# Kernel optimization log

Hardware: AMD Instinct MI355X
Metric: run time of the kernel (lower is better)

## Reference

```python
import jax, jax.numpy as jnp
import numpy as np

B, T, C, H = 4, 2048, 1024, 16
D = C // H  # head_dim = 64


def setup_inputs() -> dict:
    key = jax.random.key(0)
    k1, k2, k3, k4 = jax.random.split(key, 4)
    x = jax.random.normal(k1, (B, T, C), dtype=jnp.float32)
    # realistic padding: each sequence has length in [T//2, T]
    lengths = jax.random.randint(k4, (B,), T // 2, T + 1)
    padding_mask = jnp.arange(T)[None, :] < lengths[:, None]  # True = keep
    # weights stored [in, out] (equivalent to torch Linear weight transposed)
    w_qkv = jax.random.normal(k2, (C, 3 * C), dtype=jnp.float32) * (C ** -0.5)
    w_out = jax.random.normal(k3, (C, C), dtype=jnp.float32) * (C ** -0.5)
    b_out = jnp.zeros((C,), dtype=jnp.float32)
    return {"x": x, "padding_mask": padding_mask, "w_qkv": w_qkv, "w_out": w_out, "b_out": b_out}


def reference(x, padding_mask, w_qkv, w_out, b_out):
    scale = D ** -0.5
    qkv = x @ w_qkv  # [B,T,3C]
    q, k, v = jnp.split(qkv, 3, axis=-1)

    def split_heads(t):
        return t.reshape(B, T, H, D).transpose(0, 2, 1, 3)  # [B,H,T,D]

    q, k, v = split_heads(q), split_heads(k), split_heads(v)
    attn = jnp.einsum("bhqd,bhkd->bhqk", q, k) * scale  # [B,H,T,T]
    mask = padding_mask[:, None, None, :]  # [B,1,1,T]
    attn = jnp.where(mask, attn, jnp.finfo(attn.dtype).min)
    attn = jax.nn.softmax(attn, axis=-1)
    # dropout is identity in eval mode
    out = jnp.einsum("bhqk,bhkd->bhqd", attn, v)  # [B,H,T,D]
    out = out.transpose(0, 2, 1, 3).reshape(B, T, C)
    return out @ w_out + b_out
```

## Files before the change

### kernel.cpp

```cpp
#include <hip/hip_runtime.h>
#include <hip/hip_bf16.h>

#define Bb 4
#define Tt 2048
#define Cc 1024
#define Hh 16

typedef unsigned short u16;
typedef __attribute__((ext_vector_type(8))) __bf16 bf16x8;
typedef __attribute__((ext_vector_type(4))) float  f32x4;

__device__ __forceinline__ u16 f2bf_hw(float f) {
    __bf16 h = (__bf16)f;
    return *(u16*)&h;
}

__device__ __forceinline__ unsigned cvt_pk_bf16(float a, float b) {
    unsigned r;
    asm("v_cvt_pk_bf16_f32 %0, %1, %2" : "=v"(r) : "v"(a), "v"(b));
    return r;
}

__device__ __forceinline__ float fexp2(float x) {
#if __has_builtin(__builtin_amdgcn_exp2f)
    return __builtin_amdgcn_exp2f(x);
#else
    return __expf(x * 0.6931471805599453f);
#endif
}

__device__ __forceinline__ void gld_lds16(const void* g, void* l) {
    __builtin_amdgcn_global_load_lds(
        (__attribute__((address_space(1))) void*)(g),
        (__attribute__((address_space(3))) void*)(l),
        16, 0, 0);
}

__device__ __forceinline__ f32x4 mfma16(bf16x8 a, bf16x8 b, f32x4 c) {
    return __builtin_amdgcn_mfma_f32_16x16x32_bf16(a, b, c, 0, 0, 0);
}

__global__ void cast_f32_bf16(const float* __restrict__ in, u16* __restrict__ out, int n4) {
    int i = blockIdx.x * 256 + threadIdx.x;
    if (i < n4) {
        float4 v = ((const float4*)in)[i];
        uint2 o;
        o.x = cvt_pk_bf16(v.x, v.y);
        o.y = cvt_pk_bf16(v.z, v.w);
        ((uint2*)out)[i] = o;
    }
}

__global__ void castT_f32_bf16(const float* __restrict__ in, u16* __restrict__ out,
                               int K, int N, int scaleN, float sv) {
    __shared__ float Ls[64][65];
    const int n0 = blockIdx.x * 64, k0 = blockIdx.y * 64;
    const int t = threadIdx.x;
    #pragma unroll
    for (int s = 0; s < 4; ++s) {
        int idx = t + 256 * s;
        int r   = idx >> 4;
        int c4  = (idx & 15) * 4;
        float4 v = *(const float4*)&in[(size_t)(k0 + r) * N + n0 + c4];
        Ls[r][c4 + 0] = v.x; Ls[r][c4 + 1] = v.y;
        Ls[r][c4 + 2] = v.z; Ls[r][c4 + 3] = v.w;
    }
    __syncthreads();
    #pragma unroll
    for (int s = 0; s < 2; ++s) {
        int idx = t + 256 * s;
        int n   = idx >> 3;
        int kc  = (idx & 7) * 8;
        const float sc = (n0 + n < scaleN) ? sv : 1.0f;
        alignas(16) u16 tmp[8];
        #pragma unroll
        for (int i = 0; i < 8; ++i) tmp[i] = f2bf_hw(Ls[kc + i][n] * sc);
        *(uint4*)&out[(size_t)(n0 + n) * K + k0 + kc] = *(const uint4*)tmp;
    }
}

__global__ void repack_frags(const u16* __restrict__ qkv,
                             u16* __restrict__ kx, u16* __restrict__ vx) {
    __shared__ u16 Kt[64 * 80];
    __shared__ u16 Vt[64 * 80];
    const int t = threadIdx.x;
    const int ch = blockIdx.x, bh = blockIdx.y, b = bh >> 4, h = bh & 15;
    const int kc = ch * 64;

    #pragma unroll
    for (int u = 0; u < 2; ++u) {
        int id = t + 256 * u;
        int key = id >> 3, c8 = id & 7;
        const size_t row = (size_t)(b * Tt + kc + key) * (3 * Cc) + h * 64 + c8 * 8;
        *(uint4*)&Kt[key * 80 + c8 * 8] = *(const uint4*)&qkv[row + Cc];
        *(uint4*)&Vt[key * 80 + c8 * 8] = *(const uint4*)&qkv[row + 2 * Cc];
    }
    __syncthreads();

    const size_t obase = (size_t)(bh * 32 + ch) * 4096;
    #pragma unroll
    for (int u = 0; u < 2; ++u) {
        int id = t + 256 * u;
        int lane = id & 63, ks = (id >> 6) & 1, jt = id >> 7;
        int l16 = lane & 15, quad = lane >> 4;
        uint4 kv = *(const uint4*)&Kt[(16 * jt + l16) * 80 + 32 * ks + quad * 8];
        *(uint4*)&kx[obase + (size_t)(jt * 2 + ks) * 512 + lane * 8] = kv;
        alignas(16) u16 tmp[8];
        #pragma unroll
        for (int j = 0; j < 8; ++j)
            tmp[j] = Vt[(32 * ks + quad * 8 + j) * 80 + 16 * jt + l16];
        *(uint4*)&vx[obase + (size_t)(jt * 2 + ks) * 512 + lane * 8] = *(const uint4*)tmp;
    }
}

__global__ __launch_bounds__(256, 3) void gemm_bt_bf16(
    const u16* __restrict__ A, const u16* __restrict__ Bt,
    const float* __restrict__ bias,
    u16* __restrict__ outB, float* __restrict__ outF,
    int M, int N, int K)
{
    __shared__ u16 As[128 * 32];
    __shared__ u16 Bs[128 * 32];
    const int t = threadIdx.x;
    const int w = t >> 6, lane = t & 63;
    const int quad = lane >> 4, l16 = lane & 15;
    const int wr = w >> 1, wc = w & 1;
    const int m0 = blockIdx.y * 128, n0 = blockIdx.x * 128;

    int aoff[4], boff[4];
    #pragma unroll
    for (int i = 0; i < 4; ++i) {
        int rA = 64 * wr + 16 * i + l16;
        aoff[i] = rA * 32 + ((quad ^ ((rA >> 1) & 3)) * 8);
        int rB = 64 * wc + 16 * i + l16;
        boff[i] = rB * 32 + ((quad ^ ((rB >> 1) & 3)) * 8);
    }

    f32x4 acc[4][4] = {};

    for (int k0 = 0; k0 < K; k0 += 32) {
        __syncthreads();
        #pragma unroll
        for (int u = 0; u < 2; ++u) {
            const int i   = 2 * w + u;
            const int row = 16 * i + (lane >> 2);
            const int c   = (lane & 3) ^ ((row >> 1) & 3);
            gld_lds16(A  + (size_t)(m0 + row) * K + k0 + c * 8, (void*)(As + i * 512 + lane * 8));
            gld_lds16(Bt + (size_t)(n0 + row) * K + k0 + c * 8, (void*)(Bs + i * 512 + lane * 8));
        }
        asm volatile("s_waitcnt vmcnt(0)" ::: "memory");
        __syncthreads();

        bf16x8 af[4], bfr[4];
        #pragma unroll
        for (int i = 0; i < 4; ++i) af[i]  = *(const bf16x8*)&As[aoff[i]];
        #pragma unroll
        for (int j = 0; j < 4; ++j) bfr[j] = *(const bf16x8*)&Bs[boff[j]];
        #pragma unroll
        for (int i = 0; i < 4; ++i)
            #pragma unroll
            for (int j = 0; j < 4; ++j)
                acc[i][j] = mfma16(af[i], bfr[j], acc[i][j]);
    }

    const int rbase = m0 + 64 * wr + quad * 4;
    const int cbase = n0 + 64 * wc + l16;
    if (outF) {
        float bv[4];
        #pragma unroll
        for (int j = 0; j < 4; ++j) bv[j] = bias[cbase + 16 * j];
        #pragma unroll
        for (int i = 0; i < 4; ++i)
            #pragma unroll
            for (int r = 0; r < 4; ++r) {
                size_t ro = (size_t)(rbase + 16 * i + r) * N;
                #pragma unroll
                for (int j = 0; j < 4; ++j)
                    outF[ro + cbase + 16 * j] = acc[i][j][r] + bv[j];
            }
    } else {
        #pragma unroll
        for (int i = 0; i < 4; ++i)
            #pragma unroll
            for (int r = 0; r < 4; ++r) {
                size_t ro = (size_t)(rbase + 16 * i + r) * N;
                #pragma unroll
                for (int j = 0; j < 4; ++j)
                    outB[ro + cbase + 16 * j] = f2bf_hw(acc[i][j][r]);
            }
    }
}

__global__ __launch_bounds__(64, 2) void attn_mfma(
    const u16* __restrict__ qkv, const u16* __restrict__ kx, const u16* __restrict__ vx,
    const int* __restrict__ mask, u16* __restrict__ outO)
{
    __shared__ u16 Ps[64 * 68];

    const int lane = threadIdx.x;
    const int quad = lane >> 4, l16 = lane & 15;
    const int bh = blockIdx.x, qt = blockIdx.y, b = bh >> 4, h = bh & 15;

    int sum = 0;
    {
        const int4* mp = (const int4*)(mask + b * Tt) + lane * 8;
        #pragma unroll
        for (int i = 0; i < 8; ++i) { int4 m4 = mp[i]; sum += m4.x + m4.y + m4.z + m4.w; }
        #pragma unroll
        for (int off = 1; off < 64; off <<= 1) sum += __shfl_xor(sum, off);
    }
    const int L = sum;

    const int q0 = qt * 64;
    bf16x8 qf[4][2];
    #pragma unroll
    for (int qq = 0; qq < 4; ++qq) {
        const u16* qp = qkv + (size_t)(b * Tt + q0 + 16 * qq + l16) * (3 * Cc) + h * 64 + quad * 8;
        qf[qq][0] = *(const bf16x8*)(qp);
        qf[qq][1] = *(const bf16x8*)(qp + 32);
    }

    f32x4 oacc[4][4] = {};
    f32x4 lacc[4]    = {};
    const __bf16 onebf = (__bf16)1.0f;
    const bf16x8 ones  = {onebf, onebf, onebf, onebf, onebf, onebf, onebf, onebf};

    const int nfull = L >> 6;
    const int nch   = (L + 63) >> 6;
    const size_t fb = (size_t)bh * 32 * 4096 + lane * 8;

    uint4 kf[4][2];
    #pragma unroll
    for (int jt = 0; jt < 4; ++jt)
        #pragma unroll
        for (int ks = 0; ks < 2; ++ks)
            kf[jt][ks] = *(const uint4*)&kx[fb + (size_t)(jt * 2 + ks) * 512];

    for (int ch = 0; ch < nch; ++ch) {
        uint4 vf[4][2];
        #pragma unroll
        for (int jt = 0; jt < 4; ++jt)
            #pragma unroll
            for (int ks = 0; ks < 2; ++ks)
                vf[jt][ks] = *(const uint4*)&vx[fb + (size_t)ch * 4096 + (size_t)(jt * 2 + ks) * 512];

        #pragma unroll
        for (int qq = 0; qq < 4; ++qq) {
            f32x4 st[4];
            #pragma unroll
            for (int jt = 0; jt < 4; ++jt) {
                f32x4 z = {0.f, 0.f, 0.f, 0.f};
                z = mfma16(*(const bf16x8*)&kf[jt][0], qf[qq][0], z);
                st[jt] = mfma16(*(const bf16x8*)&kf[jt][1], qf[qq][1], z);
            }
            uint2 pk[4];
            if (ch < nfull) {
                #pragma unroll
                for (int jt = 0; jt < 4; ++jt) {
                    pk[jt].x = cvt_pk_bf16(fexp2(st[jt][0]), fexp2(st[jt][1]));
                    pk[jt].y = cvt_pk_bf16(fexp2(st[jt][2]), fexp2(st[jt][3]));
                }
            } else {
                const int kc = ch * 64;
                #pragma unroll
                for (int jt = 0; jt < 4; ++jt) {
                    const int kb = kc + 16 * jt + quad * 4;
                    float e[4];
                    #pragma unroll
                    for (int r = 0; r < 4; ++r)
                        e[r] = (kb + r < L) ? fexp2(st[jt][r]) : 0.f;
                    pk[jt].x = cvt_pk_bf16(e[0], e[1]);
                    pk[jt].y = cvt_pk_bf16(e[2], e[3]);
                }
            }
            #pragma unroll
            for (int jt = 0; jt < 4; ++jt)
                *(uint2*)&Ps[(16 * qq + l16) * 68 + 16 * jt + quad * 4] = pk[jt];
        }

        {
            const int chn = (ch + 1 < nch) ? ch + 1 : ch;
            #pragma unroll
            for (int jt = 0; jt < 4; ++jt)
                #pragma unroll
                for (int ks = 0; ks < 2; ++ks)
                    kf[jt][ks] = *(const uint4*)&kx[fb + (size_t)chn * 4096 + (size_t)(jt * 2 + ks) * 512];
        }

        #pragma unroll
        for (int qq = 0; qq < 4; ++qq) {
            #pragma unroll
            for (int ks = 0; ks < 2; ++ks) {
                const u16* pr = &Ps[(16 * qq + l16) * 68 + 32 * ks + quad * 8];
                uint2 pa = *(const uint2*)pr;
                uint2 pb = *(const uint2*)(pr + 4);
                uint4 comb = {pa.x, pa.y, pb.x, pb.y};
                bf16x8 pf = *(const bf16x8*)&comb;
                #pragma unroll
                for (int dt = 0; dt < 4; ++dt)
                    oacc[qq][dt] = mfma16(pf, *(const bf16x8*)&vf[dt][ks], oacc[qq][dt]);
                lacc[qq] = mfma16(pf, ones, lacc[qq]);
            }
        }
    }

    #pragma unroll
    for (int qq = 0; qq < 4; ++qq)
        #pragma unroll
        for (int r = 0; r < 4; ++r) {
            const float inv = 1.f / lacc[qq][r];
            const size_t ro = (size_t)(b * Tt + q0 + 16 * qq + quad * 4 + r) * Cc + h * 64 + l16;
            #pragma unroll
            for (int dt = 0; dt < 4; ++dt)
                outO[ro + 16 * dt] = f2bf_hw(oacc[qq][dt][r] * inv);
        }
}

extern "C" void kernel_launch(void* const* d_in, const int* in_sizes, int n_in,
                              void* d_out, int out_size, void* d_ws, size_t ws_size,
                              hipStream_t stream) {
    const float* x     = (const float*)d_in[0];
    const int*   mask  = (const int*)  d_in[1];
    const float* w_qkv = (const float*)d_in[2];
    const float* w_out = (const float*)d_in[3];
    const float* b_out = (const float*)d_in[4];
    float*       outp  = (float*)d_out;

    const int M = Bb * Tt;
    char* ws = (char*)d_ws;
    u16* xb     = (u16*)(ws);
    u16* wqkvT  = (u16*)(ws + (16u << 20));
    u16* woutT  = (u16*)(ws + (22u << 20));
    u16* qkv    = (u16*)(ws + (24u << 20));
    u16* kx     = (u16*)(ws + (72u << 20));
    u16* vx     = (u16*)(ws + (88u << 20));
    u16* attnO  = (u16*)(ws);

    const float c2 = 0.18033688011112042f;

    cast_f32_bf16<<<(M * Cc / 4 + 255) / 256, 256, 0, stream>>>(x, xb, M * Cc / 4);
    castT_f32_bf16<<<dim3(3 * Cc / 64, Cc / 64), 256, 0, stream>>>(w_qkv, wqkvT, Cc, 3 * Cc, Cc, c2);
    castT_f32_bf16<<<dim3(Cc / 64, Cc / 64), 256, 0, stream>>>(w_out, woutT, Cc, Cc, 0, 1.0f);

    gemm_bt_bf16<<<dim3(3 * Cc / 128, M / 128), 256, 0, stream>>>(
        xb, wqkvT, nullptr, qkv, nullptr, M, 3 * Cc, Cc);

    repack_frags<<<dim3(Tt / 64, Bb * Hh), 256, 0, stream>>>(qkv, kx, vx);

    attn_mfma<<<dim3(Bb * Hh, Tt / 64), 64, 0, stream>>>(qkv, kx, vx, mask, attnO);

    gemm_bt_bf16<<<dim3(Cc / 128, M / 128), 256, 0, stream>>>(
        attnO, woutT, b_out, nullptr, outp, M, Cc, Cc);
}
```

Measured before the change: 268.7 us.

## Add 256x256-tile pipelined GEMM kernel for the QKV projection

Adds a new GEMM kernel for the QKV projection. It uses 256x256 output tiles, 512 threads, and double-buffered LDS staging through global-to-LDS loads with XOR swizzling. Each K-step is split into four MFMA phases that interleave the next tile's loads, use s_setprio around the MFMA bursts, and apply a grouped workgroup remap for L2 locality. The larger tile raises data reuse and overlaps memory with compute. In exchange it uses 128KB of LDS and many accumulator registers, which limits occupancy, and it launches only 12x32 workgroups.

```diff
diff --git a/kernel.cpp b/kernel.cpp
--- a/kernel.cpp
+++ b/kernel.cpp
@@ -191,6 +191,135 @@
     }
 }
 
+#define PH_PRE()  do { __builtin_amdgcn_s_barrier();                        \
+                       asm volatile("s_waitcnt lgkmcnt(0)" ::: "memory");   \
+                       __builtin_amdgcn_sched_barrier(0);                   \
+                       __builtin_amdgcn_s_setprio(1); } while (0)
+#define PH_POST() do { __builtin_amdgcn_s_setprio(0);                       \
+                       __builtin_amdgcn_s_barrier(); } while (0)
+
+__global__ __launch_bounds__(512, 2) void gemm_bt_256(
+    const u16* __restrict__ A, const u16* __restrict__ Bt,
+    u16* __restrict__ out, int M, int N, int K)
+{
+    __shared__ u16 sm[65536];
+    const int t = threadIdx.x;
+    const int w = t >> 6, lane = t & 63;
+    const int quad = lane >> 4, l16 = lane & 15;
+    const int wm = w >> 2, wn = w & 3;
+
+    const int gx   = gridDim.x;
+    const int nwg  = gx * gridDim.y;
+    const int orig = blockIdx.y * gx + blockIdx.x;
+    const int wg   = (orig & 7) * (nwg >> 3) + (orig >> 3);
+    const int bn = wg % gx, bm = wg / gx;
+    const int m0 = bm << 8, n0 = bn << 8;
+    const int NKT = K >> 6;
+
+    const int l8r   = lane >> 3;
+    const int g_log = (lane & 7) ^ l8r;
+    const u16* sAp[4]; const u16* sBp[4];
+    #pragma unroll
+    for (int u = 0; u < 4; ++u) {
+        const int gi = w * 4 + u;
+        sAp[u] = A  + (size_t)(m0 + gi * 8 + l8r) * K + g_log * 8;
+        sBp[u] = Bt + (size_t)(n0 + gi * 8 + l8r) * K + g_log * 8;
+    }
+    const int dst0 = w * 2048 + lane * 8;
+
+    auto STAGE = [&](int tt, int u, int p) {
+        const int tc = (tt < NKT) ? tt : (NKT - 1);
+        const size_t ko = (size_t)tc << 6;
+        u16* d = sm + p * 32768 + dst0 + u * 512;
+        gld_lds16(sAp[u] + ko, d);
+        gld_lds16(sBp[u] + ko, d + 16384);
+    };
+
+    const int x7   = l16 & 7;
+    const int rowA = (wm * 128 + l16) * 64;
+    const int rowB = (wn * 64  + l16) * 64;
+    const int sw0  = (quad ^ x7) * 8;
+    const int sw1  = ((4 + quad) ^ x7) * 8;
+    const int a00 = rowA + sw0, a01 = rowA + sw1;
+    const int b00 = rowB + sw0, b01 = rowB + sw1;
+
+    f32x4 acc[8][4] = {};
+
+    STAGE(0, 0, 0); STAGE(0, 1, 0); STAGE(0, 2, 0); STAGE(0, 3, 0);
+    STAGE(1, 0, 1);
+    asm volatile("s_waitcnt vmcnt(2)" ::: "memory");
+    __builtin_amdgcn_s_barrier();
+
+    for (int kt = 0; kt < NKT; ++kt) {
+        const int p = kt & 1;
+        const u16* LA = sm + p * 32768;
+        const u16* LB = LA + 16384;
+        bf16x8 ar0[4], ar1[4], br0[4], br1[4];
+
+        #pragma unroll
+        for (int m = 0; m < 4; ++m) ar0[m] = *(const bf16x8*)&LA[a00 + m * 1024];
+        #pragma unroll
+        for (int n = 0; n < 4; ++n) br0[n] = *(const bf16x8*)&LB[b00 + n * 1024];
+        STAGE(kt + 1, 1, p ^ 1);
+        PH_PRE();
+        #pragma unroll
+        for (int m = 0; m < 4; ++m)
+            #pragma unroll
+            for (int n = 0; n < 4; ++n)
+                acc[m][n] = mfma16(ar0[m], br0[n], acc[m][n]);
+        PH_POST();
+
+        #pragma unroll
+        for (int m = 0; m < 4; ++m) ar1[m] = *(const bf16x8*)&LA[a00 + (4 + m) * 1024];
+        #pragma unroll
+        for (int n = 0; n < 4; ++n) br1[n] = *(const bf16x8*)&LB[b01 + n * 1024];
+        STAGE(kt + 1, 2, p ^ 1);
+        PH_PRE();
+        #pragma unroll
+        for (int m = 0; m < 4; ++m)
+            #pragma unroll
+            for (int n = 0; n < 4; ++n)
+                acc[4 + m][n] = mfma16(ar1[m], br0[n], acc[4 + m][n]);
+        PH_POST();
+
+        #pragma unroll
+        for (int m = 0; m < 4; ++m) ar0[m] = *(const bf16x8*)&LA[a01 + m * 1024];
+        #pragma unroll
+        for (int m = 0; m < 4; ++m) ar1[m] = *(const bf16x8*)&LA[a01 + (4 + m) * 1024];
+        STAGE(kt + 1, 3, p ^ 1);
+        PH_PRE();
+        #pragma unroll
+        for (int m = 0; m < 4; ++m)
+            #pragma unroll
+            for (int n = 0; n < 4; ++n)
+                acc[m][n] = mfma16(ar0[m], br1[n], acc[m][n]);
+        PH_POST();
+
+        STAGE(kt + 2, 0, p);
+        PH_PRE();
+        #pragma unroll
+        for (int m = 0; m < 4; ++m)
+            #pragma unroll
+            for (int n = 0; n < 4; ++n)
+                acc[4 + m][n] = mfma16(ar1[m], br1[n], acc[4 + m][n]);
+        __builtin_amdgcn_s_setprio(0);
+        asm volatile("s_waitcnt vmcnt(2)" ::: "memory");
+        __builtin_amdgcn_s_barrier();
+    }
+
+    const int rb = m0 + wm * 128 + quad * 4;
+    const int cb = n0 + wn * 64 + l16;
+    #pragma unroll
+    for (int m = 0; m < 8; ++m)
+        #pragma unroll
+        for (int r = 0; r < 4; ++r) {
+            const size_t ro = (size_t)(rb + m * 16 + r) * N;
+            #pragma unroll
+            for (int n = 0; n < 4; ++n)
+                out[ro + cb + n * 16] = f2bf_hw(acc[m][n][r]);
+        }
+}
+
 __global__ __launch_bounds__(64, 2) void attn_mfma(
     const u16* __restrict__ qkv, const u16* __restrict__ kx, const u16* __restrict__ vx,
     const int* __restrict__ mask, u16* __restrict__ outO)
@@ -342,8 +471,8 @@
     castT_f32_bf16<<<dim3(3 * Cc / 64, Cc / 64), 256, 0, stream>>>(w_qkv, wqkvT, Cc, 3 * Cc, Cc, c2);
     castT_f32_bf16<<<dim3(Cc / 64, Cc / 64), 256, 0, stream>>>(w_out, woutT, Cc, Cc, 0, 1.0f);
 
-    gemm_bt_bf16<<<dim3(3 * Cc / 128, M / 128), 256, 0, stream>>>(
-        xb, wqkvT, nullptr, qkv, nullptr, M, 3 * Cc, Cc);
+    gemm_bt_256<<<dim3(3 * Cc / 256, M / 256), 512, 0, stream>>>(
+        xb, wqkvT, qkv, M, 3 * Cc, Cc);
 
     repack_frags<<<dim3(Tt / 64, Bb * Hh), 256, 0, stream>>>(qkv, kx, vx);
 
```

After: 263.4 us. 1.02x faster.

## Share K/V tiles across four waves via double-buffered LDS in attention

Applied to the files above, without the earlier changes.

The attention kernel now runs four wavefronts per block, each handling 64 queries (256 queries per block). K and V chunks are staged once per block into a double-buffered LDS region with direct global-to-LDS loads, and the next chunk is prefetched while the current one is processed. This is meant to cut redundant global and L2 traffic for K/V, since the previous design had each 64-query wave fetch the fragments on its own. In exchange it adds a block-wide barrier per chunk, uses more LDS per block, and launches fewer blocks.

```diff
diff --git a/kernel.cpp b/kernel.cpp
--- a/kernel.cpp
+++ b/kernel.cpp
@@ -191,15 +191,17 @@
     }
 }
 
-__global__ __launch_bounds__(64, 2) void attn_mfma(
+__global__ __launch_bounds__(256, 2) void attn_mfma4(
     const u16* __restrict__ qkv, const u16* __restrict__ kx, const u16* __restrict__ vx,
     const int* __restrict__ mask, u16* __restrict__ outO)
 {
-    __shared__ u16 Ps[64 * 68];
-
-    const int lane = threadIdx.x;
+    __shared__ u16 KVs[2][8192];
+    __shared__ u16 Pss[4][64 * 68];
+
+    const int t = threadIdx.x;
+    const int w = t >> 6, lane = t & 63;
     const int quad = lane >> 4, l16 = lane & 15;
-    const int bh = blockIdx.x, qt = blockIdx.y, b = bh >> 4, h = bh & 15;
+    const int bh = blockIdx.x, qb = blockIdx.y, b = bh >> 4, h = bh & 15;
 
     int sum = 0;
     {
@@ -211,7 +213,7 @@
     }
     const int L = sum;
 
-    const int q0 = qt * 64;
+    const int q0 = qb * 256 + w * 64;
     bf16x8 qf[4][2];
     #pragma unroll
     for (int qq = 0; qq < 4; ++qq) {
@@ -227,22 +229,42 @@
 
     const int nfull = L >> 6;
     const int nch   = (L + 63) >> 6;
-    const size_t fb = (size_t)bh * 32 * 4096 + lane * 8;
-
-    uint4 kf[4][2];
-    #pragma unroll
-    for (int jt = 0; jt < 4; ++jt)
-        #pragma unroll
-        for (int ks = 0; ks < 2; ++ks)
-            kf[jt][ks] = *(const uint4*)&kx[fb + (size_t)(jt * 2 + ks) * 512];
+    const size_t cb0 = (size_t)bh * 32 * 4096;
+    u16* Pw = Pss[w];
+
+    {
+        const u16* ksrc = kx + cb0;
+        const u16* vsrc = vx + cb0;
+        gld_lds16(ksrc + t * 8,        &KVs[0][t * 8]);
+        gld_lds16(ksrc + 2048 + t * 8, &KVs[0][2048 + t * 8]);
+        gld_lds16(vsrc + t * 8,        &KVs[0][4096 + t * 8]);
+        gld_lds16(vsrc + 2048 + t * 8, &KVs[0][6144 + t * 8]);
+    }
+    __syncthreads();
 
     for (int ch = 0; ch < nch; ++ch) {
-        uint4 vf[4][2];
+        const int p = ch & 1;
+
+        {
+            const int cc = (ch + 1 < nch) ? ch + 1 : ch;
+            const u16* ksrc = kx + cb0 + (size_t)cc * 4096;
+            const u16* vsrc = vx + cb0 + (size_t)cc * 4096;
+            u16* d = KVs[p ^ 1];
+            gld_lds16(ksrc + t * 8,        d + t * 8);
+            gld_lds16(ksrc + 2048 + t * 8, d + 2048 + t * 8);
+            gld_lds16(vsrc + t * 8,        d + 4096 + t * 8);
+            gld_lds16(vsrc + 2048 + t * 8, d + 6144 + t * 8);
+        }
+
+        const u16* Kb = KVs[p];
+        const u16* Vb = KVs[p] + 4096;
+
+        bf16x8 kf[4][2];
         #pragma unroll
         for (int jt = 0; jt < 4; ++jt)
             #pragma unroll
             for (int ks = 0; ks < 2; ++ks)
-                vf[jt][ks] = *(const uint4*)&vx[fb + (size_t)ch * 4096 + (size_t)(jt * 2 + ks) * 512];
+                kf[jt][ks] = *(const bf16x8*)&Kb[(jt * 2 + ks) * 512 + lane * 8];
 
         #pragma unroll
         for (int qq = 0; qq < 4; ++qq) {
@@ -250,8 +272,8 @@
             #pragma unroll
             for (int jt = 0; jt < 4; ++jt) {
                 f32x4 z = {0.f, 0.f, 0.f, 0.f};
-                z = mfma16(*(const bf16x8*)&kf[jt][0], qf[qq][0], z);
-                st[jt] = mfma16(*(const bf16x8*)&kf[jt][1], qf[qq][1], z);
+                z = mfma16(kf[jt][0], qf[qq][0], z);
+                st[jt] = mfma16(kf[jt][1], qf[qq][1], z);
             }
             uint2 pk[4];
             if (ch < nfull) {
@@ -275,33 +297,33 @@
             }
             #pragma unroll
             for (int jt = 0; jt < 4; ++jt)
-                *(uint2*)&Ps[(16 * qq + l16) * 68 + 16 * jt + quad * 4] = pk[jt];
-        }
-
-        {
-            const int chn = (ch + 1 < nch) ? ch + 1 : ch;
-            #pragma unroll
-            for (int jt = 0; jt < 4; ++jt)
-                #pragma unroll
-                for (int ks = 0; ks < 2; ++ks)
-                    kf[jt][ks] = *(const uint4*)&kx[fb + (size_t)chn * 4096 + (size_t)(jt * 2 + ks) * 512];
-        }
+                *(uint2*)&Pw[(16 * qq + l16) * 68 + 16 * jt + quad * 4] = pk[jt];
+        }
+
+        bf16x8 vf[4][2];
+        #pragma unroll
+        for (int dt = 0; dt < 4; ++dt)
+            #pragma unroll
+            for (int ks = 0; ks < 2; ++ks)
+                vf[dt][ks] = *(const bf16x8*)&Vb[(dt * 2 + ks) * 512 + lane * 8];
 
         #pragma unroll
         for (int qq = 0; qq < 4; ++qq) {
             #pragma unroll
             for (int ks = 0; ks < 2; ++ks) {
-                const u16* pr = &Ps[(16 * qq + l16) * 68 + 32 * ks + quad * 8];
+                const u16* pr = &Pw[(16 * qq + l16) * 68 + 32 * ks + quad * 8];
                 uint2 pa = *(const uint2*)pr;
                 uint2 pb = *(const uint2*)(pr + 4);
                 uint4 comb = {pa.x, pa.y, pb.x, pb.y};
                 bf16x8 pf = *(const bf16x8*)&comb;
                 #pragma unroll
                 for (int dt = 0; dt < 4; ++dt)
-                    oacc[qq][dt] = mfma16(pf, *(const bf16x8*)&vf[dt][ks], oacc[qq][dt]);
+                    oacc[qq][dt] = mfma16(pf, vf[dt][ks], oacc[qq][dt]);
                 lacc[qq] = mfma16(pf, ones, lacc[qq]);
             }
         }
+
+        __syncthreads();
     }
 
     #pragma unroll
@@ -347,7 +369,7 @@
 
     repack_frags<<<dim3(Tt / 64, Bb * Hh), 256, 0, stream>>>(qkv, kx, vx);
 
-    attn_mfma<<<dim3(Bb * Hh, Tt / 64), 64, 0, stream>>>(qkv, kx, vx, mask, attnO);
+    attn_mfma4<<<dim3(Bb * Hh, Tt / 256), 256, 0, stream>>>(qkv, kx, vx, mask, attnO);
 
     gemm_bt_bf16<<<dim3(Cc / 128, M / 128), 256, 0, stream>>>(
         attnO, woutT, b_out, nullptr, outp, M, Cc, Cc);
```

Measured after the change: 268.5 us. About the same (-0.1%).
